# Performance work log

Hardware: AMD Instinct MI355X
Metric: run time of the kernel (lower is better)

The kernel has to match this reference:

```python
import jax, jax.numpy as jnp
import numpy as np

B, H, G, N, D = 1, 32, 64, 128, 128   # batch, heads, blocks, block_len, head_dim
S = 256                               # sketch dim (multiple of 16)
BIT_PACK = 8


def setup_inputs() -> dict:
    key = jax.random.key(0)
    k1, k2, k3 = jax.random.split(key, 3)
    data = jax.random.normal(k1, (B, H, G, N, D), dtype=jnp.float32)
    # binary per-channel outlier mask, float {0,1}, shape matches data.shape[:3] + (D,)
    outlier_mask = jax.random.randint(k2, (B, H, G, D), 0, 2).astype(jnp.float32)
    # proj_dir_quant = proj_dir_score.T -> shape (S, D)
    proj_dir_quant = jax.random.normal(k3, (S, D), dtype=jnp.float32)
    return {"data": data, "outlier_mask": outlier_mask, "proj_dir_quant": proj_dir_quant}


def _pack_bits(sketch):
    # sketch: (..., S). Reshape to (..., S//8, 8), threshold at 0, pack sign bits into uint8.
    x = sketch.reshape(*sketch.shape[:-1], -1, BIT_PACK)
    enc = (2 ** jnp.arange(BIT_PACK, dtype=jnp.int32))  # [1,2,4,...,128]
    packed = ((x > 0).astype(jnp.int32) * enc).sum(axis=-1)  # max 255, fits uint8
    return packed.astype(jnp.uint8)


def reference(data, outlier_mask, proj_dir_quant):
    s = proj_dir_quant.shape[0]
    m = outlier_mask[..., None, :]                     # (B,H,G,1,D) broadcast over tokens
    key_outlier = data * m
    key_inlier = data * (1.0 - m)
    # '...nd,sd->...ns' : sign-random-projection sketch
    sk_outlier = jnp.einsum('bhgnd,sd->bhgns', key_outlier, proj_dir_quant)
    sk_inlier = jnp.einsum('bhgnd,sd->bhgns', key_inlier, proj_dir_quant)
    hash_inlier = _pack_bits(sk_inlier)                # (B,H,G,N,S//8)
    hash_outlier = _pack_bits(sk_outlier)[..., : s // 16]  # (B,H,G,N,S//16)
    return (hash_inlier, hash_outlier)
```

## Files before the change

kernel.cpp:

```cpp
#include <hip/hip_runtime.h>

#define NB_HG 2048
#define DIM_N 128
#define DIM_D 128

__global__ __launch_bounds__(256)
void qjl_sketch_kernel(const float* __restrict__ data,
                       const float* __restrict__ mask,
                       const float* __restrict__ proj,
                       int* __restrict__ out)
{
    __shared__ float Xt[DIM_D * DIM_N];
    __shared__ int   cidx[DIM_D];
    __shared__ int   wcnt[2];

    const int type = blockIdx.x;
    const int hg   = blockIdx.y;
    const int tid  = threadIdx.x;

    bool sel = false; int pos = 0, w = 0;
    if (tid < 128) {
        const float m = mask[hg * DIM_D + tid];
        sel = (type == 2) ? (m != 0.0f) : (m == 0.0f);
        const unsigned long long bal = __ballot(sel);
        const int lane = tid & 63;
        w = tid >> 6;
        if (lane == 0) wcnt[w] = __popcll(bal);
        pos = __popcll(bal & ((1ull << lane) - 1ull));
    }
    __syncthreads();
    if (sel) cidx[pos + (w ? wcnt[0] : 0)] = tid;
    __syncthreads();
    const int K = wcnt[0] + wcnt[1];

    {
        const int ci = tid & 127;
        const int nh = tid >> 7;
        if (ci < K) {
            const int   dg = cidx[ci];
            const float* Xs = data + (size_t)hg * (DIM_N * DIM_D) + dg;
            const int   pcs = 4 * (ci & 7);
            float* row = &Xt[ci * DIM_N];
            #pragma unroll
            for (int g = 0; g < 16; ++g) {
                const int n0 = nh * 64 + g * 4;
                float4 v;
                v.x = Xs[(size_t)(n0 + 0) * DIM_D];
                v.y = Xs[(size_t)(n0 + 1) * DIM_D];
                v.z = Xs[(size_t)(n0 + 2) * DIM_D];
                v.w = Xs[(size_t)(n0 + 3) * DIM_D];
                *reinterpret_cast<float4*>(&row[n0 ^ pcs]) = v;
            }
        }
    }
    __syncthreads();

    const int tn = tid & 15;
    const int ts = tid >> 4;
    const int C0 = 4 * tn;
    const int s0 = ((type == 1) ? 128 : 0) + ts * 8;
    const float* pbase = proj + (size_t)s0 * DIM_D;

    float acc[8][8];
    #pragma unroll
    for (int j = 0; j < 8; ++j)
        #pragma unroll
        for (int i = 0; i < 8; ++i) acc[j][i] = 0.0f;

    #pragma unroll 2
    for (int ci = 0; ci < K; ++ci) {
        const int dg = cidx[ci];
        float b[8];
        #pragma unroll
        for (int j = 0; j < 8; ++j)
            b[j] = pbase[(size_t)j * DIM_D + dg];

        const int P = C0 ^ (4 * (ci & 7));
        const float* r = &Xt[ci * DIM_N + P];
        const float4 q0 = *reinterpret_cast<const float4*>(r);
        const float4 q1 = *reinterpret_cast<const float4*>(r + 64);

        #pragma unroll
        for (int j = 0; j < 8; ++j) {
            const float bv = b[j];
            acc[j][0] = fmaf(bv, q0.x, acc[j][0]);
            acc[j][1] = fmaf(bv, q0.y, acc[j][1]);
            acc[j][2] = fmaf(bv, q0.z, acc[j][2]);
            acc[j][3] = fmaf(bv, q0.w, acc[j][3]);
            acc[j][4] = fmaf(bv, q1.x, acc[j][4]);
            acc[j][5] = fmaf(bv, q1.y, acc[j][5]);
            acc[j][6] = fmaf(bv, q1.z, acc[j][6]);
            acc[j][7] = fmaf(bv, q1.w, acc[j][7]);
        }
    }

    const size_t inl_total = (size_t)NB_HG * DIM_N * 32;
    #pragma unroll
    for (int i = 0; i < 8; ++i) {
        int byte = 0;
        #pragma unroll
        for (int j = 0; j < 8; ++j)
            if (acc[j][i] > 0.0f) byte |= (1 << j);
        const int n = (i < 4) ? (C0 + i) : (64 + C0 + (i - 4));
        size_t idx;
        if (type == 2)
            idx = inl_total + ((size_t)hg * DIM_N + n) * 16 + ts;
        else
            idx = ((size_t)hg * DIM_N + n) * 32 + (type == 1 ? 16 : 0) + ts;
        out[idx] = byte;
    }
}

extern "C" void kernel_launch(void* const* d_in, const int* in_sizes, int n_in,
                              void* d_out, int out_size, void* d_ws, size_t ws_size,
                              hipStream_t stream) {
    const float* data = (const float*)d_in[0];
    const float* mask = (const float*)d_in[1];
    const float* proj = (const float*)d_in[2];
    int* out = (int*)d_out;

    dim3 grid(3, NB_HG);
    qjl_sketch_kernel<<<grid, 256, 0, stream>>>(data, mask, proj, out);
}
```

Before: 229.0 us.

## Halve shared tile via two-pass staging and pre-transpose projection for vector loads

Shrinks the shared-memory tile from 128 to 64 channel rows and stages the selected channels in up to two passes, which should let more blocks fit per CU. It also adds a small kernel that transposes the projection matrix into the workspace, so each thread loads its 8 sketch coefficients with two float4 loads instead of 8 strided scalar loads. This costs an extra kernel launch, extra barriers, and a serialized second staging pass when more than 64 channels are selected.

```diff
diff --git a/kernel.cpp b/kernel.cpp
--- a/kernel.cpp
+++ b/kernel.cpp
@@ -3,14 +3,25 @@
 #define NB_HG 2048
 #define DIM_N 128
 #define DIM_D 128
+#define DIM_S 256
 
+
+__global__ void transpose_proj_kernel(const float* __restrict__ proj,
+                                      float* __restrict__ projT)
+{
+    const int d = blockIdx.x;
+    const int s = threadIdx.x;
+    projT[d * DIM_S + s] = proj[s * DIM_D + d];
+}
+
+template<bool TP>
 __global__ __launch_bounds__(256)
 void qjl_sketch_kernel(const float* __restrict__ data,
                        const float* __restrict__ mask,
-                       const float* __restrict__ proj,
+                       const float* __restrict__ pmat,
                        int* __restrict__ out)
 {
-    __shared__ float Xt[DIM_D * DIM_N];
+    __shared__ float Xt[64 * DIM_N];
     __shared__ int   cidx[DIM_D];
     __shared__ int   wcnt[2];
 
@@ -33,33 +44,10 @@
     __syncthreads();
     const int K = wcnt[0] + wcnt[1];
 
-    {
-        const int ci = tid & 127;
-        const int nh = tid >> 7;
-        if (ci < K) {
-            const int   dg = cidx[ci];
-            const float* Xs = data + (size_t)hg * (DIM_N * DIM_D) + dg;
-            const int   pcs = 4 * (ci & 7);
-            float* row = &Xt[ci * DIM_N];
-            #pragma unroll
-            for (int g = 0; g < 16; ++g) {
-                const int n0 = nh * 64 + g * 4;
-                float4 v;
-                v.x = Xs[(size_t)(n0 + 0) * DIM_D];
-                v.y = Xs[(size_t)(n0 + 1) * DIM_D];
-                v.z = Xs[(size_t)(n0 + 2) * DIM_D];
-                v.w = Xs[(size_t)(n0 + 3) * DIM_D];
-                *reinterpret_cast<float4*>(&row[n0 ^ pcs]) = v;
-            }
-        }
-    }
-    __syncthreads();
-
     const int tn = tid & 15;
     const int ts = tid >> 4;
     const int C0 = 4 * tn;
     const int s0 = ((type == 1) ? 128 : 0) + ts * 8;
-    const float* pbase = proj + (size_t)s0 * DIM_D;
 
     float acc[8][8];
     #pragma unroll
@@ -67,31 +55,73 @@
         #pragma unroll
         for (int i = 0; i < 8; ++i) acc[j][i] = 0.0f;
 
-    #pragma unroll 2
-    for (int ci = 0; ci < K; ++ci) {
-        const int dg = cidx[ci];
-        float b[8];
-        #pragma unroll
-        for (int j = 0; j < 8; ++j)
-            b[j] = pbase[(size_t)j * DIM_D + dg];
+    const int cl_s = tid & 63;
+    const int nh   = tid >> 6;
+    const int pcs  = 4 * (cl_s & 7);
+    float* srow = &Xt[cl_s * DIM_N];
 
-        const int P = C0 ^ (4 * (ci & 7));
-        const float* r = &Xt[ci * DIM_N + P];
-        const float4 q0 = *reinterpret_cast<const float4*>(r);
-        const float4 q1 = *reinterpret_cast<const float4*>(r + 64);
+    auto STAGE = [&](int base, int kp) {
+        if (cl_s < kp) {
+            const int dg = cidx[base + cl_s];
+            const float* Xs = data + (size_t)hg * (DIM_N * DIM_D) + dg;
+            #pragma unroll
+            for (int g = 0; g < 8; ++g) {
+                const int n0 = nh * 32 + g * 4;
+                float4 v;
+                v.x = Xs[(size_t)(n0 + 0) * DIM_D];
+                v.y = Xs[(size_t)(n0 + 1) * DIM_D];
+                v.z = Xs[(size_t)(n0 + 2) * DIM_D];
+                v.w = Xs[(size_t)(n0 + 3) * DIM_D];
+                *reinterpret_cast<float4*>(&srow[n0 ^ pcs]) = v;
+            }
+        }
+    };
 
-        #pragma unroll
-        for (int j = 0; j < 8; ++j) {
-            const float bv = b[j];
-            acc[j][0] = fmaf(bv, q0.x, acc[j][0]);
-            acc[j][1] = fmaf(bv, q0.y, acc[j][1]);
-            acc[j][2] = fmaf(bv, q0.z, acc[j][2]);
-            acc[j][3] = fmaf(bv, q0.w, acc[j][3]);
-            acc[j][4] = fmaf(bv, q1.x, acc[j][4]);
-            acc[j][5] = fmaf(bv, q1.y, acc[j][5]);
-            acc[j][6] = fmaf(bv, q1.z, acc[j][6]);
-            acc[j][7] = fmaf(bv, q1.w, acc[j][7]);
+    auto COMPUTE = [&](int base, int kp) {
+        #pragma unroll 2
+        for (int cl = 0; cl < kp; ++cl) {
+            const int dg = cidx[base + cl];
+            float bv[8];
+            if (TP) {
+                const float* pr = pmat + (size_t)dg * DIM_S + s0;
+                const float4 b0 = *reinterpret_cast<const float4*>(pr);
+                const float4 b1 = *reinterpret_cast<const float4*>(pr + 4);
+                bv[0]=b0.x; bv[1]=b0.y; bv[2]=b0.z; bv[3]=b0.w;
+                bv[4]=b1.x; bv[5]=b1.y; bv[6]=b1.z; bv[7]=b1.w;
+            } else {
+                #pragma unroll
+                for (int j = 0; j < 8; ++j)
+                    bv[j] = pmat[(size_t)(s0 + j) * DIM_D + dg];
+            }
+
+            const int P = C0 ^ (4 * (cl & 7));
+            const float* r = &Xt[cl * DIM_N + P];
+            const float4 q0 = *reinterpret_cast<const float4*>(r);
+            const float4 q1 = *reinterpret_cast<const float4*>(r + 64);
+
+            #pragma unroll
+            for (int j = 0; j < 8; ++j) {
+                acc[j][0] = fmaf(bv[j], q0.x, acc[j][0]);
+                acc[j][1] = fmaf(bv[j], q0.y, acc[j][1]);
+                acc[j][2] = fmaf(bv[j], q0.z, acc[j][2]);
+                acc[j][3] = fmaf(bv[j], q0.w, acc[j][3]);
+                acc[j][4] = fmaf(bv[j], q1.x, acc[j][4]);
+                acc[j][5] = fmaf(bv[j], q1.y, acc[j][5]);
+                acc[j][6] = fmaf(bv[j], q1.z, acc[j][6]);
+                acc[j][7] = fmaf(bv[j], q1.w, acc[j][7]);
+            }
         }
+    };
+
+    const int k0 = (K < 64) ? K : 64;
+    STAGE(0, k0);
+    __syncthreads();
+    COMPUTE(0, k0);
+    if (K > 64) {
+        __syncthreads();
+        STAGE(64, K - 64);
+        __syncthreads();
+        COMPUTE(64, K - 64);
     }
 
     const size_t inl_total = (size_t)NB_HG * DIM_N * 32;
@@ -120,5 +150,12 @@
     int* out = (int*)d_out;
 
     dim3 grid(3, NB_HG);
-    qjl_sketch_kernel<<<grid, 256, 0, stream>>>(data, mask, proj, out);
+    const size_t tp_bytes = (size_t)DIM_D * DIM_S * sizeof(float);
+    if (ws_size >= tp_bytes) {
+        float* projT = (float*)d_ws;
+        transpose_proj_kernel<<<DIM_D, DIM_S, 0, stream>>>(proj, projT);
+        qjl_sketch_kernel<true><<<grid, 256, 0, stream>>>(data, mask, projT, out);
+    } else {
+        qjl_sketch_kernel<false><<<grid, 256, 0, stream>>>(data, mask, proj, out);
+    }
 }
```

Measured after the change: 202.9 us. 1.13x faster.
